# Optimization experiments

Hardware: AMD Instinct MI355X
Metric: run time of the kernel (lower is better)

Reference implementation:

```python
import jax, jax.numpy as jnp
import numpy as np

NUM_HEADS = 16
EPS = 1e-6
ROPE_THETA = 10000.0


def _rmsnorm_fp32(x, w):
    # RMSNorm computed in fp32, scale by learned weight (per head_dim)
    xf = x.astype(jnp.float32)
    var = jnp.mean(xf * xf, axis=-1, keepdims=True)
    return (xf * jax.lax.rsqrt(var + EPS) * w.astype(jnp.float32)).astype(x.dtype)


def _rope_3d_angles(T, H, W, head_dim):
    # split head_dim across (t,h,w) axes; all parts even
    dh = 2 * ((head_dim // 3) // 2)
    dw = dh
    dt = head_dim - dh - dw

    def axis_ang(L, d):
        inv = 1.0 / (ROPE_THETA ** (jnp.arange(0, d, 2, dtype=jnp.float32) / d))
        return jnp.arange(L, dtype=jnp.float32)[:, None] * inv[None, :]  # [L, d//2]

    at = axis_ang(T, dt)  # [T, dt/2]
    ah = axis_ang(H, dh)  # [H, dh/2]
    aw = axis_ang(W, dw)  # [W, dw/2]
    # broadcast to [T,H,W, head_dim//2] then flatten to [N, head_dim//2]
    at_g = jnp.broadcast_to(at[:, None, None, :], (T, H, W, dt // 2))
    ah_g = jnp.broadcast_to(ah[None, :, None, :], (T, H, W, dh // 2))
    aw_g = jnp.broadcast_to(aw[None, None, :, :], (T, H, W, dw // 2))
    ang = jnp.concatenate([at_g, ah_g, aw_g], axis=-1).reshape(T * H * W, head_dim // 2)
    return jnp.cos(ang), jnp.sin(ang)


def _apply_rope(x, cos, sin):
    # x: [B,Hh,N,D]; cos/sin: [N, D/2]; interleaved complex-pair rotation
    xr = x[..., 0::2]
    xi = x[..., 1::2]
    c = cos[None, None, :, :]
    s = sin[None, None, :, :]
    out_r = xr * c - xi * s
    out_i = xr * s + xi * c
    return jnp.stack([out_r, out_i], axis=-1).reshape(x.shape)


def setup_inputs() -> dict:
    key = jax.random.key(0)
    ks = jax.random.split(key, 7)
    dim, hd = 2048, 128
    x = jax.random.normal(ks[0], (1, 2048, dim), dtype=jnp.float32)
    qkv_w = jax.random.normal(ks[1], (3 * dim, dim), dtype=jnp.float32) * (dim ** -0.5)
    qkv_b = jax.random.normal(ks[2], (3 * dim,), dtype=jnp.float32) * 0.02
    proj_w = jax.random.normal(ks[3], (dim, dim), dtype=jnp.float32) * (dim ** -0.5)
    proj_b = jax.random.normal(ks[4], (dim,), dtype=jnp.float32) * 0.02
    q_norm_w = jnp.ones((hd,), dtype=jnp.float32)
    k_norm_w = jnp.ones((hd,), dtype=jnp.float32)
    return {"x": x, "qkv_w": qkv_w, "qkv_b": qkv_b, "proj_w": proj_w,
            "proj_b": proj_b, "q_norm_w": q_norm_w, "k_norm_w": k_norm_w,
            "t_dim": 8, "h_dim": 16, "w_dim": 16}


def reference(x, qkv_w, qkv_b, proj_w, proj_b, q_norm_w, k_norm_w, t_dim, h_dim, w_dim):
    B, N, C = x.shape
    Hh = NUM_HEADS
    D = C // Hh
    scale = D ** -0.5
    # QKV projection (torch Linear: x @ W.T + b)
    qkv = x @ qkv_w.T + qkv_b                      # [B,N,3C]
    qkv = qkv.reshape(B, N, 3, Hh, D).transpose(2, 0, 3, 1, 4)  # [3,B,Hh,N,D]
    q, k, v = qkv[0], qkv[1], qkv[2]
    q = _rmsnorm_fp32(q, q_norm_w)
    k = _rmsnorm_fp32(k, k_norm_w)
    cos, sin = _rope_3d_angles(t_dim, h_dim, w_dim, D)
    q = _apply_rope(q, cos, sin)
    k = _apply_rope(k, cos, sin)
    # SDPA (non-causal)
    scores = jnp.einsum('bhqd,bhkd->bhqk', q, k) * scale
    attn = jax.nn.softmax(scores, axis=-1)
    out = jnp.einsum('bhqk,bhkd->bhqd', attn, v)   # [B,Hh,N,D]
    out = out.transpose(0, 2, 1, 3).reshape(B, N, C)
    return out @ proj_w.T + proj_b
```

## Files before the change

kernel.cpp:

```cpp
#include <hip/hip_runtime.h>
#include <hip/hip_bf16.h>
#include <cstdint>
#include <cstddef>

typedef __attribute__((ext_vector_type(8))) short bf16x8;
typedef __attribute__((ext_vector_type(4))) float f32x4;
typedef __attribute__((ext_vector_type(16))) float f32x16;

#define AS1 __attribute__((address_space(1)))
#define AS3 __attribute__((address_space(3)))

__device__ __forceinline__ void gload_lds16(const void* g, void* l) {
  __builtin_amdgcn_global_load_lds((const AS1 void*)g, (AS3 void*)l, 16, 0, 0);
}

__device__ __forceinline__ unsigned short f2bf(float x) {
  __hip_bfloat16 h = __float2bfloat16(x);
  return __builtin_bit_cast(unsigned short, h);
}
__device__ __forceinline__ float bf2f(unsigned short u) {
  return __builtin_bit_cast(float, (unsigned int)u << 16);
}
__device__ __forceinline__ unsigned cvtpk(float a, float b) {
  unsigned r;
  asm("v_cvt_pk_bf16_f32 %0, %1, %2" : "=v"(r) : "v"(a), "v"(b));
  return r;
}
__device__ __forceinline__ void pswap(unsigned& x, unsigned& y) {
  asm volatile("v_permlane32_swap_b32 %0, %1" : "+v"(x), "+v"(y));
}

__global__ __launch_bounds__(256) void k_cvt_bf16(const float* __restrict__ in,
                                                  unsigned short* __restrict__ out,
                                                  int n4) {
  int i = blockIdx.x * 256 + threadIdx.x;
  const int stride = gridDim.x * 256;
  for (; i < n4; i += stride) {
    float4 v = reinterpret_cast<const float4*>(in)[i];
    ushort4 o;
    o.x = f2bf(v.x); o.y = f2bf(v.y); o.z = f2bf(v.z); o.w = f2bf(v.w);
    reinterpret_cast<ushort4*>(out)[i] = o;
  }
}

__global__ __launch_bounds__(256) void k_rope_tab(float* __restrict__ cosT,
                                                  float* __restrict__ sinT,
                                                  const int* __restrict__ hdim,
                                                  const int* __restrict__ wdim) {
  int idx = blockIdx.x * 256 + threadIdx.x;
  if (idx >= 2048 * 64) return;
  const int n = idx >> 6, j = idx & 63;
  const int H = *hdim, W = *wdim;
  const int w = n % W;
  const int rem = n / W;
  const int h = rem % H;
  const int t = rem / H;
  float pos, i2, d;
  if (j < 22)      { pos = (float)t; i2 = (float)(2 * j);        d = 44.f; }
  else if (j < 43) { pos = (float)h; i2 = (float)(2 * (j - 22)); d = 42.f; }
  else             { pos = (float)w; i2 = (float)(2 * (j - 43)); d = 42.f; }
  const float ang = pos * powf(10000.0f, -i2 / d);
  cosT[idx] = cosf(ang);
  sinT[idx] = sinf(ang);
}

__global__ __launch_bounds__(256, 2) void k_gemmQKV(const unsigned short* __restrict__ A,
                                                    const unsigned short* __restrict__ B,
                                                    const float* __restrict__ bias,
                                                    unsigned short* __restrict__ C,
                                                    int M, int N, int K) {
  __shared__ __align__(16) char lds[81920];
  const int tid = threadIdx.x;
  const int lane = tid & 63;
  const int wid = tid >> 6;
  const int wr = wid >> 1, wc = wid & 1;

  const int xcd = blockIdx.x & 7;
  const int t = blockIdx.x >> 3;
  const int bx = xcd * 4 + (t & 3);
  const int by = t >> 2;
  const int row0 = by * 128, col0 = bx * 192;
  const int NT = K >> 6;

  auto stageA = [&](int grow0, int kcol0, char* slot) {
#pragma unroll
    for (int r = 0; r < 2; ++r) {
      const int off = r * 4096 + tid * 16;
      const int pair = off >> 7;
      const int un = (off & 127) ^ ((pair & 7) << 4);
      const int grow = pair * 2 + (un >> 6);
      gload_lds16(A + (size_t)(grow0 + grow) * K + kcol0 + ((un & 63) >> 1),
                  slot + r * 4096 + wid * 1024);
    }
  };
  auto stageB = [&](int grow0, int kcol0, char* slot) {
#pragma unroll
    for (int r = 0; r < 3; ++r) {
      const int off = r * 4096 + tid * 16;
      const int pair = off >> 7;
      const int un = (off & 127) ^ ((pair & 7) << 4);
      const int grow = pair * 2 + (un >> 6);
      gload_lds16(B + (size_t)(grow0 + grow) * K + kcol0 + ((un & 63) >> 1),
                  slot + r * 4096 + wid * 1024);
    }
  };
  auto frag = [&](const char* slot, int r, int kb) -> bf16x8 {
    return *reinterpret_cast<const bf16x8*>(
        slot + (r >> 1) * 128 + ((((r & 1) << 6) + kb) ^ (((r >> 1) & 7) << 4)));
  };

  f32x4 acc[4][6];
#pragma unroll
  for (int i = 0; i < 4; ++i)
#pragma unroll
    for (int j = 0; j < 6; ++j) acc[i][j] = (f32x4){0.f, 0.f, 0.f, 0.f};

  stageA(row0, 0,  lds);
  stageB(col0, 0,  lds + 16384);
  stageA(row0, 32, lds + 8192);
  stageB(col0, 32, lds + 28672);
  asm volatile("s_waitcnt vmcnt(5)" ::: "memory");
  __builtin_amdgcn_s_barrier();

  const int kb = (lane >> 4) << 4;
  for (int j = 0; j < NT; ++j) {
    const int b = j & 1, bp = b ^ 1;
    const char* base = lds + b * 40960;
    char* pbase = lds + bp * 40960;
    const bool pf = (j + 1 < NT);
    const int kn = (j + 1) * 64;
    bf16x8 af[4], bq[6];

#pragma unroll
    for (int fr = 0; fr < 4; ++fr) af[fr] = frag(base, wr * 64 + fr * 16 + (lane & 15), kb);
#pragma unroll
    for (int fc = 0; fc < 6; ++fc) bq[fc] = frag(base + 16384, wc * 96 + fc * 16 + (lane & 15), kb);
    if (pf) { stageA(row0, kn, pbase); stageB(col0, kn, pbase + 16384); }
    if (pf) asm volatile("s_waitcnt vmcnt(5)" ::: "memory");
    else    asm volatile("s_waitcnt vmcnt(0)" ::: "memory");
    __builtin_amdgcn_s_barrier();
    __builtin_amdgcn_s_setprio(1);
#pragma unroll
    for (int fr = 0; fr < 4; ++fr)
#pragma unroll
      for (int fc = 0; fc < 6; ++fc)
        acc[fr][fc] = __builtin_amdgcn_mfma_f32_16x16x32_bf16(af[fr], bq[fc], acc[fr][fc], 0, 0, 0);
    __builtin_amdgcn_s_setprio(0);

#pragma unroll
    for (int fr = 0; fr < 4; ++fr) af[fr] = frag(base + 8192, wr * 64 + fr * 16 + (lane & 15), kb);
#pragma unroll
    for (int fc = 0; fc < 6; ++fc) bq[fc] = frag(base + 28672, wc * 96 + fc * 16 + (lane & 15), kb);
    if (pf) { stageA(row0, kn + 32, pbase + 8192); stageB(col0, kn + 32, pbase + 28672); }
    if (pf) asm volatile("s_waitcnt vmcnt(5)" ::: "memory");
    __builtin_amdgcn_s_barrier();
    __builtin_amdgcn_s_setprio(1);
#pragma unroll
    for (int fr = 0; fr < 4; ++fr)
#pragma unroll
      for (int fc = 0; fc < 6; ++fc)
        acc[fr][fc] = __builtin_amdgcn_mfma_f32_16x16x32_bf16(af[fr], bq[fc], acc[fr][fc], 0, 0, 0);
    __builtin_amdgcn_s_setprio(0);
  }

#pragma unroll
  for (int fr = 0; fr < 4; ++fr)
#pragma unroll
    for (int fc = 0; fc < 6; ++fc) {
      const int col = col0 + wc * 96 + fc * 16 + (lane & 15);
      const float bv = bias[col];
#pragma unroll
      for (int jj = 0; jj < 4; ++jj) {
        const int row = row0 + wr * 64 + fr * 16 + (lane >> 4) * 4 + jj;
        C[(size_t)row * N + col] = f2bf(acc[fr][fc][jj] + bv);
      }
    }
}

__global__ __launch_bounds__(256, 2) void k_gemmProj(const unsigned short* __restrict__ A,
                                                     const unsigned short* __restrict__ B,
                                                     float* __restrict__ Cp,
                                                     int M, int N, int K, int KS) {
  __shared__ __align__(16) char lds[65536];
  const int tid = threadIdx.x;
  const int lane = tid & 63;
  const int wid = tid >> 6;
  const int wr = wid >> 1, wc = wid & 1;
  const int row0 = blockIdx.y * 128;
  const int col0 = blockIdx.x * 128;
  const int k0 = blockIdx.z * KS;
  const int NT = KS >> 6;

  auto stageS = [&](const unsigned short* src, int grow0, int kcol0, char* slot) {
#pragma unroll
    for (int r = 0; r < 2; ++r) {
      const int off = r * 4096 + tid * 16;
      const int pair = off >> 7;
      const int un = (off & 127) ^ ((pair & 7) << 4);
      const int grow = pair * 2 + (un >> 6);
      gload_lds16(src + (size_t)(grow0 + grow) * K + kcol0 + ((un & 63) >> 1),
                  slot + r * 4096 + wid * 1024);
    }
  };
  auto frag = [&](const char* slot, int r, int kb) -> bf16x8 {
    return *reinterpret_cast<const bf16x8*>(
        slot + (r >> 1) * 128 + ((((r & 1) << 6) + kb) ^ (((r >> 1) & 7) << 4)));
  };

  f32x4 acc[4][4];
#pragma unroll
  for (int i = 0; i < 4; ++i)
#pragma unroll
    for (int j = 0; j < 4; ++j) acc[i][j] = (f32x4){0.f, 0.f, 0.f, 0.f};

  stageS(A, row0, k0,      lds);
  stageS(B, col0, k0,      lds + 16384);
  stageS(A, row0, k0 + 32, lds + 8192);
  stageS(B, col0, k0 + 32, lds + 24576);
  asm volatile("s_waitcnt vmcnt(4)" ::: "memory");
  __builtin_amdgcn_s_barrier();

  const int kb = (lane >> 4) << 4;
  for (int j = 0; j < NT; ++j) {
    const int b = j & 1, bp = b ^ 1;
    const char* base = lds + b * 32768;
    char* pbase = lds + bp * 32768;
    const bool pf = (j + 1 < NT);
    const int kn = k0 + (j + 1) * 64;
    bf16x8 af[4], bq[4];

#pragma unroll
    for (int fr = 0; fr < 4; ++fr) af[fr] = frag(base, wr * 64 + fr * 16 + (lane & 15), kb);
#pragma unroll
    for (int fc = 0; fc < 4; ++fc) bq[fc] = frag(base + 16384, wc * 64 + fc * 16 + (lane & 15), kb);
    if (pf) { stageS(A, row0, kn, pbase); stageS(B, col0, kn, pbase + 16384); }
    if (pf) asm volatile("s_waitcnt vmcnt(4)" ::: "memory");
    else    asm volatile("s_waitcnt vmcnt(0)" ::: "memory");
    __builtin_amdgcn_s_barrier();
    __builtin_amdgcn_s_setprio(1);
#pragma unroll
    for (int fr = 0; fr < 4; ++fr)
#pragma unroll
      for (int fc = 0; fc < 4; ++fc)
        acc[fr][fc] = __builtin_amdgcn_mfma_f32_16x16x32_bf16(af[fr], bq[fc], acc[fr][fc], 0, 0, 0);
    __builtin_amdgcn_s_setprio(0);

#pragma unroll
    for (int fr = 0; fr < 4; ++fr) af[fr] = frag(base + 8192, wr * 64 + fr * 16 + (lane & 15), kb);
#pragma unroll
    for (int fc = 0; fc < 4; ++fc) bq[fc] = frag(base + 24576, wc * 64 + fc * 16 + (lane & 15), kb);
    if (pf) { stageS(A, row0, kn + 32, pbase + 8192); stageS(B, col0, kn + 32, pbase + 24576); }
    if (pf) asm volatile("s_waitcnt vmcnt(4)" ::: "memory");
    __builtin_amdgcn_s_barrier();
    __builtin_amdgcn_s_setprio(1);
#pragma unroll
    for (int fr = 0; fr < 4; ++fr)
#pragma unroll
      for (int fc = 0; fc < 4; ++fc)
        acc[fr][fc] = __builtin_amdgcn_mfma_f32_16x16x32_bf16(af[fr], bq[fc], acc[fr][fc], 0, 0, 0);
    __builtin_amdgcn_s_setprio(0);
  }

  float* Cz = Cp + (size_t)blockIdx.z * M * N;
#pragma unroll
  for (int fr = 0; fr < 4; ++fr)
#pragma unroll
    for (int fc = 0; fc < 4; ++fc) {
      const int col = col0 + wc * 64 + fc * 16 + (lane & 15);
#pragma unroll
      for (int jj = 0; jj < 4; ++jj) {
        const int row = row0 + wr * 64 + fr * 16 + (lane >> 4) * 4 + jj;
        Cz[(size_t)row * N + col] = acc[fr][fc][jj];
      }
    }
}

__global__ __launch_bounds__(256) void k_addbias(const float* __restrict__ Cp,
                                                 const float* __restrict__ bias,
                                                 float* __restrict__ out) {
  const int i = blockIdx.x * 256 + threadIdx.x;
  const float4 a = reinterpret_cast<const float4*>(Cp)[i];
  const float4 b = reinterpret_cast<const float4*>(Cp + 2048ull * 2048)[i];
  const float4 bv = reinterpret_cast<const float4*>(bias)[i & 511];
  float4 o;
  o.x = a.x + b.x + bv.x; o.y = a.y + b.y + bv.y;
  o.z = a.z + b.z + bv.z; o.w = a.w + b.w + bv.w;
  reinterpret_cast<float4*>(out)[i] = o;
}

__global__ __launch_bounds__(256) void k_qk_post(const unsigned short* __restrict__ qkv,
                                                 const float* __restrict__ qw,
                                                 const float* __restrict__ kw,
                                                 const float* __restrict__ cosT,
                                                 const float* __restrict__ sinT,
                                                 unsigned short* __restrict__ qo,
                                                 unsigned short* __restrict__ ko) {
  const int lane = threadIdx.x & 63;
  const int wid = threadIdx.x >> 6;
  const int pair = blockIdx.x * 4 + wid;
  const int n = pair >> 4, h = pair & 15;
  const float c = cosT[n * 64 + lane];
  const float s = sinT[n * 64 + lane];
#pragma unroll
  for (int sq = 0; sq < 2; ++sq) {
    const unsigned short* src = qkv + (size_t)n * 6144 + sq * 2048 + h * 128;
    const unsigned int vp = reinterpret_cast<const unsigned int*>(src)[lane];
    const float vx = bf2f((unsigned short)(vp & 0xffff));
    const float vy = bf2f((unsigned short)(vp >> 16));
    float ss = vx * vx + vy * vy;
#pragma unroll
    for (int m = 1; m < 64; m <<= 1) ss += __shfl_xor(ss, m, 64);
    const float r = rsqrtf(ss * (1.0f / 128.0f) + 1e-6f);
    float2 wv = reinterpret_cast<const float2*>(sq == 0 ? qw : kw)[lane];
    const float xr = vx * r * wv.x;
    const float xi = vy * r * wv.y;
    float orr = xr * c - xi * s;
    float oi  = xr * s + xi * c;
    if (sq == 0) { orr *= 0.08838834764831845f; oi *= 0.08838834764831845f; }
    unsigned short* dst = (sq == 0 ? qo : ko) + ((size_t)h * 2048 + n) * 128 + 2 * lane;
    const unsigned int pk = (unsigned int)f2bf(orr) | ((unsigned int)f2bf(oi) << 16);
    *reinterpret_cast<unsigned int*>(dst) = pk;
  }
}

__global__ __launch_bounds__(256) void k_v_tr(const unsigned short* __restrict__ qkv,
                                              unsigned short* __restrict__ vt2) {
  __shared__ __align__(16) unsigned short tile[64][136];
  const int h = blockIdx.y;
  const int n0 = blockIdx.x * 64;
  const int t = threadIdx.x;
  {
    const int row = t >> 2;
    const int c0 = (t & 3) * 32;
    const unsigned short* src = qkv + (size_t)(n0 + row) * 6144 + 4096 + h * 128 + c0;
#pragma unroll
    for (int j = 0; j < 32; j += 8)
      *reinterpret_cast<bf16x8*>(&tile[row][c0 + j]) =
          *reinterpret_cast<const bf16x8*>(src + j);
  }
  __syncthreads();
#pragma unroll
  for (int g4 = 0; g4 < 4; ++g4) {
    const int g = g4 * 256 + t;
    const int c = g >> 8;
    const int dblk = (g >> 6) & 3;
    const int p = g & 63;
    const int d = dblk * 32 + (p & 31);
    const int hi = p >> 5;
    bf16x8 o;
#pragma unroll
    for (int e = 0; e < 8; ++e) o[e] = (short)tile[c * 16 + hi * 8 + e][d];
    const size_t oidx = ((((size_t)h * 128 + (n0 >> 4) + c) * 4 + dblk) * 64 + p) * 8;
    *reinterpret_cast<bf16x8*>(vt2 + oidx) = o;
  }
}

__global__ __launch_bounds__(256) void k_fattn(const unsigned short* __restrict__ q,
                                               const unsigned short* __restrict__ k,
                                               const unsigned short* __restrict__ vt2,
                                               unsigned short* __restrict__ Onorm,
                                               float* __restrict__ lseb) {
  __shared__ __align__(16) unsigned short Ks[2][64 * 128];
  __shared__ __align__(16) unsigned short Vs[2][64 * 128];
  const int lane = threadIdx.x & 63;
  const int wid = threadIdx.x >> 6;
  const int hi2 = lane >> 5;
  const int ql = lane & 31;
  const int bid = blockIdx.x;
  const int h = bid & 15;
  const int qb = (bid >> 4) & 15;
  const int ksp = bid >> 8;
  const int q0 = qb * 128 + wid * 32;
  const int kbase = ksp * 1024;

  auto stageK = [&](int buf, int kt2) {
#pragma unroll
    for (int r = 0; r < 4; ++r) {
      const int off = r * 4096 + (wid * 64 + lane) * 16;
      const int row = off >> 8;
      const int colb = (off & 255) ^ ((row & 15) << 4);
      gload_lds16(k + ((size_t)h * 2048 + kbase + kt2 * 64 + row) * 128 + (colb >> 1),
                  (char*)Ks[buf] + r * 4096 + wid * 1024);
    }
  };
  auto stageV = [&](int buf, int kt2) {
    const unsigned short* vbase = vt2 + ((size_t)h * 128 + (kbase >> 4) + kt2 * 4) * 2048;
#pragma unroll
    for (int r = 0; r < 4; ++r)
      gload_lds16(vbase + r * 2048 + (wid * 64 + lane) * 8,
                  (char*)Vs[buf] + r * 4096 + wid * 1024);
  };

  bf16x8 qf[8];
  {
    const unsigned short* qp = q + ((size_t)h * 2048 + q0 + ql) * 128 + hi2 * 8;
#pragma unroll
    for (int c = 0; c < 8; ++c) qf[c] = *reinterpret_cast<const bf16x8*>(qp + c * 16);
  }
  f32x16 O[4];
#pragma unroll
  for (int i = 0; i < 4; ++i)
#pragma unroll
    for (int j = 0; j < 16; ++j) O[i][j] = 0.f;
  float m = -1e30f, l = 0.f;

  stageK(0, 0);
  stageV(0, 0);
  asm volatile("s_waitcnt vmcnt(0)" ::: "memory");
  __builtin_amdgcn_s_barrier();

  const int kswz = (lane & 15) << 4;
  for (int kt = 0; kt < 16; ++kt) {
    const int cur = kt & 1;
    const bool pf = (kt + 1 < 16);
    if (pf) { stageK(cur ^ 1, kt + 1); stageV(cur ^ 1, kt + 1); }

    f32x16 s0, s1;
#pragma unroll
    for (int j = 0; j < 16; ++j) { s0[j] = 0.f; s1[j] = 0.f; }
    __builtin_amdgcn_s_setprio(1);
#pragma unroll
    for (int c = 0; c < 8; ++c) {
      bf16x8 a0 = *reinterpret_cast<const bf16x8*>(
          (const char*)Ks[cur] + ql * 256 + ((c * 32 + hi2 * 16) ^ kswz));
      s0 = __builtin_amdgcn_mfma_f32_32x32x16_bf16(a0, qf[c], s0, 0, 0, 0);
    }
#pragma unroll
    for (int c = 0; c < 8; ++c) {
      bf16x8 a1 = *reinterpret_cast<const bf16x8*>(
          (const char*)Ks[cur] + (32 + ql) * 256 + ((c * 32 + hi2 * 16) ^ kswz));
      s1 = __builtin_amdgcn_mfma_f32_32x32x16_bf16(a1, qf[c], s1, 0, 0, 0);
    }
    __builtin_amdgcn_s_setprio(0);

    float mt = s0[0];
#pragma unroll
    for (int j = 1; j < 16; ++j) mt = fmaxf(mt, s0[j]);
#pragma unroll
    for (int j = 0; j < 16; ++j) mt = fmaxf(mt, s1[j]);
    mt = fmaxf(mt, __shfl_xor(mt, 32, 64));

    if (!__all(mt <= m + 8.0f)) {
      const float mn = fmaxf(m, mt);
      const float al = __expf(m - mn);
      m = mn;
      l *= al;
#pragma unroll
      for (int i = 0; i < 4; ++i)
#pragma unroll
        for (int j = 0; j < 16; ++j) O[i][j] *= al;
    }
    float rs = 0.f;
#pragma unroll
    for (int j = 0; j < 16; ++j) {
      s0[j] = __expf(s0[j] - m); rs += s0[j];
      s1[j] = __expf(s1[j] - m); rs += s1[j];
    }
    rs += __shfl_xor(rs, 32, 64);
    l += rs;

    bf16x8 pfr[4];
#pragma unroll
    for (int half = 0; half < 2; ++half) {
      const f32x16& sv = half ? s1 : s0;
      unsigned a[8];
#pragma unroll
      for (int j2 = 0; j2 < 8; ++j2) a[j2] = cvtpk(sv[2 * j2], sv[2 * j2 + 1]);
      pswap(a[0], a[2]);
      pswap(a[1], a[3]);
      pswap(a[4], a[6]);
      pswap(a[5], a[7]);
      union { uint4 u; bf16x8 v; } p0, p1;
      p0.u.x = a[0]; p0.u.y = a[1]; p0.u.z = a[2]; p0.u.w = a[3];
      p1.u.x = a[4]; p1.u.y = a[5]; p1.u.z = a[6]; p1.u.w = a[7];
      pfr[half * 2 + 0] = p0.v;
      pfr[half * 2 + 1] = p1.v;
    }

    __builtin_amdgcn_s_setprio(1);
#pragma unroll
    for (int dblk = 0; dblk < 4; ++dblk) {
#pragma unroll
      for (int c2 = 0; c2 < 4; ++c2) {
        bf16x8 va = *reinterpret_cast<const bf16x8*>(
            (const char*)Vs[cur] + ((c2 * 4 + dblk) * 64 + lane) * 16);
        O[dblk] = __builtin_amdgcn_mfma_f32_32x32x16_bf16(va, pfr[c2], O[dblk], 0, 0, 0);
      }
    }
    __builtin_amdgcn_s_setprio(0);

    if (pf) {
      asm volatile("s_waitcnt vmcnt(0)" ::: "memory");
      __builtin_amdgcn_s_barrier();
    }
  }

  const float rl = 1.0f / l;
  const int n = q0 + ql;
  unsigned short* ob = Onorm + (((size_t)(ksp * 16 + h) * 2048) + n) * 128;
#pragma unroll
  for (int dblk = 0; dblk < 4; ++dblk)
#pragma unroll
    for (int a = 0; a < 4; ++a) {
      uint2 w;
      w.x = (unsigned)f2bf(O[dblk][a * 4 + 0] * rl) | ((unsigned)f2bf(O[dblk][a * 4 + 1] * rl) << 16);
      w.y = (unsigned)f2bf(O[dblk][a * 4 + 2] * rl) | ((unsigned)f2bf(O[dblk][a * 4 + 3] * rl) << 16);
      *reinterpret_cast<uint2*>(ob + dblk * 32 + a * 8 + hi2 * 4) = w;
    }
  if (hi2 == 0)
    lseb[(size_t)(ksp * 16 + h) * 2048 + n] = m + logf(l);
}

__global__ __launch_bounds__(256) void k_merge(const unsigned short* __restrict__ Onorm,
                                               const float* __restrict__ lseb,
                                               unsigned short* __restrict__ att) {
  const int idx = blockIdx.x * 256 + threadIdx.x;
  const int n = idx >> 8;
  const int r = idx & 255;
  const int h = r >> 4;
  const int d0 = (r & 15) * 8;
  const float l0 = lseb[(size_t)h * 2048 + n];
  const float l1 = lseb[(size_t)(16 + h) * 2048 + n];
  const float M = fmaxf(l0, l1);
  float w0 = __expf(l0 - M), w1 = __expf(l1 - M);
  const float inv = 1.0f / (w0 + w1);
  w0 *= inv; w1 *= inv;
  const bf16x8 o0 = *reinterpret_cast<const bf16x8*>(
      Onorm + ((size_t)h * 2048 + n) * 128 + d0);
  const bf16x8 o1 = *reinterpret_cast<const bf16x8*>(
      Onorm + ((size_t)(16 + h) * 2048 + n) * 128 + d0);
  bf16x8 o;
#pragma unroll
  for (int e = 0; e < 8; ++e)
    o[e] = (short)f2bf(bf2f((unsigned short)o0[e]) * w0 + bf2f((unsigned short)o1[e]) * w1);
  *reinterpret_cast<bf16x8*>(att + (size_t)n * 2048 + h * 128 + d0) = o;
}

extern "C" void kernel_launch(void* const* d_in, const int* in_sizes, int n_in,
                              void* d_out, int out_size, void* d_ws, size_t ws_size,
                              hipStream_t stream) {
  (void)in_sizes; (void)n_in; (void)out_size; (void)ws_size;
  const float* x      = (const float*)d_in[0];
  const float* qkv_w  = (const float*)d_in[1];
  const float* qkv_b  = (const float*)d_in[2];
  const float* proj_w = (const float*)d_in[3];
  const float* proj_b = (const float*)d_in[4];
  const float* q_nw   = (const float*)d_in[5];
  const float* k_nw   = (const float*)d_in[6];
  const int* h_dim    = (const int*)d_in[8];
  const int* w_dim    = (const int*)d_in[9];
  float* out = (float*)d_out;

  char* ws = (char*)d_ws;
  size_t off = 0;
  auto carve = [&](size_t bytes) -> void* {
    void* p = ws + off;
    off += (bytes + 255) & ~(size_t)255;
    return p;
  };
  unsigned short* x_bf   = (unsigned short*)carve(2048ull * 2048 * 2);
  unsigned short* w1_bf  = (unsigned short*)carve(6144ull * 2048 * 2);
  unsigned short* w2_bf  = (unsigned short*)carve(2048ull * 2048 * 2);
  unsigned short* qkvb   = (unsigned short*)carve(2048ull * 6144 * 2);
  unsigned short* q_bf   = (unsigned short*)carve(16ull * 2048 * 128 * 2);
  unsigned short* k_bf   = (unsigned short*)carve(16ull * 2048 * 128 * 2);
  unsigned short* vt2_bf = (unsigned short*)carve(16ull * 2048 * 128 * 2);
  unsigned short* att_bf = (unsigned short*)carve(2048ull * 2048 * 2);
  unsigned short* on_bf  = (unsigned short*)carve(2ull * 16 * 2048 * 128 * 2);
  float*          lseb   = (float*)carve(2ull * 16 * 2048 * 4);
  float*          projp  = (float*)carve(2ull * 2048 * 2048 * 4);
  float*          cosT   = (float*)carve(2048ull * 64 * 4);
  float*          sinT   = (float*)carve(2048ull * 64 * 4);

  hipLaunchKernelGGL(k_cvt_bf16, dim3(2048), dim3(256), 0, stream, x, x_bf, 2048 * 2048 / 4);
  hipLaunchKernelGGL(k_cvt_bf16, dim3(2048), dim3(256), 0, stream, qkv_w, w1_bf, 6144 * 2048 / 4);
  hipLaunchKernelGGL(k_cvt_bf16, dim3(2048), dim3(256), 0, stream, proj_w, w2_bf, 2048 * 2048 / 4);
  hipLaunchKernelGGL(k_rope_tab, dim3(512), dim3(256), 0, stream, cosT, sinT, h_dim, w_dim);
  hipLaunchKernelGGL(k_gemmQKV, dim3(512), dim3(256), 0, stream,
                     x_bf, w1_bf, qkv_b, qkvb, 2048, 6144, 2048);
  hipLaunchKernelGGL(k_qk_post, dim3(8192), dim3(256), 0, stream,
                     qkvb, q_nw, k_nw, cosT, sinT, q_bf, k_bf);
  hipLaunchKernelGGL(k_v_tr, dim3(32, 16), dim3(256), 0, stream, qkvb, vt2_bf);
  hipLaunchKernelGGL(k_fattn, dim3(512), dim3(256), 0, stream,
                     q_bf, k_bf, vt2_bf, on_bf, lseb);
  hipLaunchKernelGGL(k_merge, dim3(2048), dim3(256), 0, stream, on_bf, lseb, att_bf);
  hipLaunchKernelGGL(k_gemmProj, dim3(16, 16, 2), dim3(256), 0, stream,
                     att_bf, w2_bf, projp, 2048, 2048, 2048, 1024);
  hipLaunchKernelGGL(k_addbias, dim3(4096), dim3(256), 0, stream, projp, proj_b, out);
}
```

Before: 177.6 us.

## Replace double-buffered K loop with 4-slot ring prefetching three stages ahead in GEMMs

```diff
diff --git a/kernel.cpp b/kernel.cpp
--- a/kernel.cpp
+++ b/kernel.cpp
@@ -80,27 +80,27 @@
   const int bx = xcd * 4 + (t & 3);
   const int by = t >> 2;
   const int row0 = by * 128, col0 = bx * 192;
-  const int NT = K >> 6;
-
-  auto stageA = [&](int grow0, int kcol0, char* slot) {
+  const int NT = K >> 5;
+
+  auto stageA = [&](int kcol0, char* slot) {
 #pragma unroll
     for (int r = 0; r < 2; ++r) {
       const int off = r * 4096 + tid * 16;
       const int pair = off >> 7;
       const int un = (off & 127) ^ ((pair & 7) << 4);
       const int grow = pair * 2 + (un >> 6);
-      gload_lds16(A + (size_t)(grow0 + grow) * K + kcol0 + ((un & 63) >> 1),
+      gload_lds16(A + (size_t)(row0 + grow) * K + kcol0 + ((un & 63) >> 1),
                   slot + r * 4096 + wid * 1024);
     }
   };
-  auto stageB = [&](int grow0, int kcol0, char* slot) {
+  auto stageB = [&](int kcol0, char* slot) {
 #pragma unroll
     for (int r = 0; r < 3; ++r) {
       const int off = r * 4096 + tid * 16;
       const int pair = off >> 7;
       const int un = (off & 127) ^ ((pair & 7) << 4);
       const int grow = pair * 2 + (un >> 6);
-      gload_lds16(B + (size_t)(grow0 + grow) * K + kcol0 + ((un & 63) >> 1),
+      gload_lds16(B + (size_t)(col0 + grow) * K + kcol0 + ((un & 63) >> 1),
                   slot + r * 4096 + wid * 1024);
     }
   };
@@ -115,45 +115,36 @@
 #pragma unroll
     for (int j = 0; j < 6; ++j) acc[i][j] = (f32x4){0.f, 0.f, 0.f, 0.f};
 
-  stageA(row0, 0,  lds);
-  stageB(col0, 0,  lds + 16384);
-  stageA(row0, 32, lds + 8192);
-  stageB(col0, 32, lds + 28672);
-  asm volatile("s_waitcnt vmcnt(5)" ::: "memory");
+#pragma unroll
+  for (int p = 0; p < 3; ++p) {
+    stageA(p * 32, lds + p * 8192);
+    stageB(p * 32, lds + 32768 + p * 12288);
+  }
+  asm volatile("s_waitcnt vmcnt(10)" ::: "memory");
   __builtin_amdgcn_s_barrier();
 
   const int kb = (lane >> 4) << 4;
   for (int j = 0; j < NT; ++j) {
-    const int b = j & 1, bp = b ^ 1;
-    const char* base = lds + b * 40960;
-    char* pbase = lds + bp * 40960;
-    const bool pf = (j + 1 < NT);
-    const int kn = (j + 1) * 64;
+    const char* baseA = lds + (j & 3) * 8192;
+    const char* baseB = lds + 32768 + (j & 3) * 12288;
     bf16x8 af[4], bq[6];
-
-#pragma unroll
-    for (int fr = 0; fr < 4; ++fr) af[fr] = frag(base, wr * 64 + fr * 16 + (lane & 15), kb);
-#pragma unroll
-    for (int fc = 0; fc < 6; ++fc) bq[fc] = frag(base + 16384, wc * 96 + fc * 16 + (lane & 15), kb);
-    if (pf) { stageA(row0, kn, pbase); stageB(col0, kn, pbase + 16384); }
-    if (pf) asm volatile("s_waitcnt vmcnt(5)" ::: "memory");
-    else    asm volatile("s_waitcnt vmcnt(0)" ::: "memory");
-    __builtin_amdgcn_s_barrier();
-    __builtin_amdgcn_s_setprio(1);
-#pragma unroll
-    for (int fr = 0; fr < 4; ++fr)
-#pragma unroll
-      for (int fc = 0; fc < 6; ++fc)
-        acc[fr][fc] = __builtin_amdgcn_mfma_f32_16x16x32_bf16(af[fr], bq[fc], acc[fr][fc], 0, 0, 0);
-    __builtin_amdgcn_s_setprio(0);
-
-#pragma unroll
-    for (int fr = 0; fr < 4; ++fr) af[fr] = frag(base + 8192, wr * 64 + fr * 16 + (lane & 15), kb);
-#pragma unroll
-    for (int fc = 0; fc < 6; ++fc) bq[fc] = frag(base + 28672, wc * 96 + fc * 16 + (lane & 15), kb);
-    if (pf) { stageA(row0, kn + 32, pbase + 8192); stageB(col0, kn + 32, pbase + 28672); }
-    if (pf) asm volatile("s_waitcnt vmcnt(5)" ::: "memory");
-    __builtin_amdgcn_s_barrier();
+#pragma unroll
+    for (int fr = 0; fr < 4; ++fr) af[fr] = frag(baseA, wr * 64 + fr * 16 + (lane & 15), kb);
+#pragma unroll
+    for (int fc = 0; fc < 6; ++fc) bq[fc] = frag(baseB, wc * 96 + fc * 16 + (lane & 15), kb);
+
+    const int jp = j + 3;
+    if (jp < NT) {
+      stageA(jp * 32, lds + (jp & 3) * 8192);
+      stageB(jp * 32, lds + 32768 + (jp & 3) * 12288);
+      asm volatile("s_waitcnt vmcnt(10)" ::: "memory");
+    } else if (j + 2 < NT) {
+      asm volatile("s_waitcnt vmcnt(5)" ::: "memory");
+    } else if (j + 1 < NT) {
+      asm volatile("s_waitcnt vmcnt(0)" ::: "memory");
+    }
+    if (j + 1 < NT) __builtin_amdgcn_s_barrier();
+
     __builtin_amdgcn_s_setprio(1);
 #pragma unroll
     for (int fr = 0; fr < 4; ++fr)
@@ -189,7 +180,7 @@
   const int row0 = blockIdx.y * 128;
   const int col0 = blockIdx.x * 128;
   const int k0 = blockIdx.z * KS;
-  const int NT = KS >> 6;
+  const int NT = KS >> 5;
 
   auto stageS = [&](const unsigned short* src, int grow0, int kcol0, char* slot) {
 #pragma unroll
@@ -213,45 +204,36 @@
 #pragma unroll
     for (int j = 0; j < 4; ++j) acc[i][j] = (f32x4){0.f, 0.f, 0.f, 0.f};
 
-  stageS(A, row0, k0,      lds);
-  stageS(B, col0, k0,      lds + 16384);
-  stageS(A, row0, k0 + 32, lds + 8192);
-  stageS(B, col0, k0 + 32, lds + 24576);
-  asm volatile("s_waitcnt vmcnt(4)" ::: "memory");
+#pragma unroll
+  for (int p = 0; p < 3; ++p) {
+    stageS(A, row0, k0 + p * 32, lds + p * 8192);
+    stageS(B, col0, k0 + p * 32, lds + 32768 + p * 8192);
+  }
+  asm volatile("s_waitcnt vmcnt(8)" ::: "memory");
   __builtin_amdgcn_s_barrier();
 
   const int kb = (lane >> 4) << 4;
   for (int j = 0; j < NT; ++j) {
-    const int b = j & 1, bp = b ^ 1;
-    const char* base = lds + b * 32768;
-    char* pbase = lds + bp * 32768;
-    const bool pf = (j + 1 < NT);
-    const int kn = k0 + (j + 1) * 64;
+    const char* baseA = lds + (j & 3) * 8192;
+    const char* baseB = lds + 32768 + (j & 3) * 8192;
     bf16x8 af[4], bq[4];
-
-#pragma unroll
-    for (int fr = 0; fr < 4; ++fr) af[fr] = frag(base, wr * 64 + fr * 16 + (lane & 15), kb);
-#pragma unroll
-    for (int fc = 0; fc < 4; ++fc) bq[fc] = frag(base + 16384, wc * 64 + fc * 16 + (lane & 15), kb);
-    if (pf) { stageS(A, row0, kn, pbase); stageS(B, col0, kn, pbase + 16384); }
-    if (pf) asm volatile("s_waitcnt vmcnt(4)" ::: "memory");
-    else    asm volatile("s_waitcnt vmcnt(0)" ::: "memory");
-    __builtin_amdgcn_s_barrier();
-    __builtin_amdgcn_s_setprio(1);
-#pragma unroll
-    for (int fr = 0; fr < 4; ++fr)
-#pragma unroll
-      for (int fc = 0; fc < 4; ++fc)
-        acc[fr][fc] = __builtin_amdgcn_mfma_f32_16x16x32_bf16(af[fr], bq[fc], acc[fr][fc], 0, 0, 0);
-    __builtin_amdgcn_s_setprio(0);
-
-#pragma unroll
-    for (int fr = 0; fr < 4; ++fr) af[fr] = frag(base + 8192, wr * 64 + fr * 16 + (lane & 15), kb);
-#pragma unroll
-    for (int fc = 0; fc < 4; ++fc) bq[fc] = frag(base + 24576, wc * 64 + fc * 16 + (lane & 15), kb);
-    if (pf) { stageS(A, row0, kn + 32, pbase + 8192); stageS(B, col0, kn + 32, pbase + 24576); }
-    if (pf) asm volatile("s_waitcnt vmcnt(4)" ::: "memory");
-    __builtin_amdgcn_s_barrier();
+#pragma unroll
+    for (int fr = 0; fr < 4; ++fr) af[fr] = frag(baseA, wr * 64 + fr * 16 + (lane & 15), kb);
+#pragma unroll
+    for (int fc = 0; fc < 4; ++fc) bq[fc] = frag(baseB, wc * 64 + fc * 16 + (lane & 15), kb);
+
+    const int jp = j + 3;
+    if (jp < NT) {
+      stageS(A, row0, k0 + jp * 32, lds + (jp & 3) * 8192);
+      stageS(B, col0, k0 + jp * 32, lds + 32768 + (jp & 3) * 8192);
+      asm volatile("s_waitcnt vmcnt(8)" ::: "memory");
+    } else if (j + 2 < NT) {
+      asm volatile("s_waitcnt vmcnt(4)" ::: "memory");
+    } else if (j + 1 < NT) {
+      asm volatile("s_waitcnt vmcnt(0)" ::: "memory");
+    }
+    if (j + 1 < NT) __builtin_amdgcn_s_barrier();
+
     __builtin_amdgcn_s_setprio(1);
 #pragma unroll
     for (int fr = 0; fr < 4; ++fr)
```

After: 179.1 us. No clear change (+0.9%).
